# Performance work log

Hardware: AMD Instinct MI355X
Metric: run time of the kernel (lower is better)

Reference implementation:

```python
import jax, jax.numpy as jnp
import numpy as np

B, N = 64, 128
SELF_DIM, AGENT_DIM = 6, 7
C = 32            # in_mlp_dims[-1] == ia_mlp_dims[-1]
GRU_H = 2 * C     # 64
DN = ('NCHW', 'OIHW', 'NCHW')


def _lin(key, out_d, in_d):
    k1, k2 = jax.random.split(key)
    s = 1.0 / np.sqrt(in_d)
    w = jax.random.uniform(k1, (out_d, in_d), minval=-s, maxval=s, dtype=jnp.float32)
    b = jax.random.uniform(k2, (out_d,), minval=-s, maxval=s, dtype=jnp.float32)
    return w, b


def setup_inputs() -> dict:
    ks = jax.random.split(jax.random.key(0), 20)
    d = {}
    d['state'] = jax.random.normal(ks[0], (B, N, SELF_DIM + AGENT_DIM), jnp.float32)
    d['w_in1'], d['b_in1'] = _lin(ks[1], 64, AGENT_DIM)
    d['w_in2'], d['b_in2'] = _lin(ks[2], C, 64)
    s1 = 1.0 / np.sqrt(C * 9)
    d['w_c1'] = jax.random.uniform(ks[3], (64, C, 3, 3), minval=-s1, maxval=s1, dtype=jnp.float32)
    d['b_c1'] = jnp.zeros((64,), jnp.float32)
    s2 = 1.0 / np.sqrt(64 * 9)
    d['w_c2'] = jax.random.uniform(ks[4], (C, 64, 3, 3), minval=-s2, maxval=s2, dtype=jnp.float32)
    d['b_c2'] = jnp.zeros((C,), jnp.float32)
    d['w_ia1'], d['b_ia1'] = _lin(ks[5], 64, C)
    d['w_ia2'], d['b_ia2'] = _lin(ks[6], C, 64)
    d['w_s1'], d['b_s1'] = _lin(ks[7], 64, C + SELF_DIM)
    d['w_s2'], d['b_s2'] = _lin(ks[8], 32, 64)
    d['w_a1'], d['b_a1'] = _lin(ks[9], 64, 64)
    d['w_a2'], d['b_a2'] = _lin(ks[10], 32, 64)
    d['w_a3'], d['b_a3'] = _lin(ks[11], 1, 32)
    d['w_z'], _ = _lin(ks[12], GRU_H, 2 * GRU_H)
    d['w_r'], _ = _lin(ks[13], GRU_H, 2 * GRU_H)
    d['w_q'], _ = _lin(ks[14], GRU_H, 2 * GRU_H)
    d['w_m1'], d['b_m1'] = _lin(ks[15], 128, GRU_H + SELF_DIM)
    d['w_m2'], d['b_m2'] = _lin(ks[16], 64, 128)
    d['w_m3'], d['b_m3'] = _lin(ks[17], 1, 64)
    return d


def _forward(state, w_in1, b_in1, w_in2, b_in2, w_c1, b_c1, w_c2, b_c2,
             w_ia1, b_ia1, w_ia2, b_ia2, w_s1, b_s1, w_s2, b_s2,
             w_a1, b_a1, w_a2, b_a2, w_a3, b_a3, w_z, w_r, w_q,
             w_m1, b_m1, w_m2, b_m2, w_m3, b_m3):
    self_state = state[:, :, :SELF_DIM]            # (B, N, 6)
    agents = state[:, :, SELF_DIM:]                # (B, N, 7)

    # input_mlp (last_relu=True)
    h = jax.nn.relu(agents @ w_in1.T + b_in1)
    in_out = jax.nn.relu(h @ w_in2.T + b_in2)      # (B, N, C)

    # ---- AFAModule: pairwise N x N construction + conv2d edge-MLP + softmax agg ----
    f = in_out.transpose(0, 2, 1)                  # (B, C, N)
    eye = jnp.eye(N, dtype=f.dtype)
    # pair[b,c,i,j] = f[b,c,i] - f[b,c,j] + f[b,c,i]*delta_ij
    pair = f[:, :, :, None] - f[:, :, None, :] + f[:, :, :, None] * eye  # (B, C, N, N)
    w = jax.lax.conv_general_dilated(pair, w_c1, (1, 1), 'SAME', dimension_numbers=DN)
    w = jax.nn.relu(w + b_c1[None, :, None, None])
    w = jax.lax.conv_general_dilated(w, w_c2, (1, 1), 'SAME', dimension_numbers=DN)
    w = w + b_c2[None, :, None, None]
    w = jax.nn.softmax(w, axis=-1)
    afa = (pair * w).sum(-1)                        # (B, C, N)
    afa = afa.reshape(B, N, C)                      # faithful to torch .view (no transpose)
    x = in_out + afa

    # ia_mlp
    h1 = jax.nn.relu(x @ w_ia1.T + b_ia1)
    ia = h1 @ w_ia2.T + b_ia2                       # (B, N, C)

    # sort_mlp
    sort_in = jnp.concatenate([ia, self_state], axis=-1)  # (B, N, C+6)
    s1 = jax.nn.relu(sort_in @ w_s1.T + b_s1)
    sort_out = s1 @ w_s2.T + b_s2                   # (B, N, 32)
    gstate = jnp.broadcast_to(jnp.mean(sort_out, 1, keepdims=True), (B, N, 32))
    sort_mlp_input = jnp.concatenate([sort_out, gstate], axis=-1)  # (B, N, 64)

    # attention scores with masked-exp normalization
    a1 = jax.nn.relu(sort_mlp_input @ w_a1.T + b_a1)
    a2 = jax.nn.relu(a1 @ w_a2.T + b_a2)
    scores = (a2 @ w_a3.T + b_a3)[..., 0]           # (B, N)
    scores_exp = jnp.exp(scores) * (scores != 0).astype(scores.dtype)
    weights = (scores_exp / jnp.sum(scores_exp, 1, keepdims=True))[..., None]
    weighted = weights * sort_mlp_input             # (B, N, 64)

    # custom conv1d GRU (kernel 1, no bias -> channel matmuls)
    gru_input = weighted.reshape(B, GRU_H, N)       # faithful to torch .view
    h0 = sort_mlp_input.transpose(0, 2, 1)          # (B, 64, N)
    hx = jnp.concatenate([h0, gru_input], axis=1)   # (B, 128, N)
    z = jax.nn.sigmoid(jnp.einsum('oc,bcn->bon', w_z, hx))
    r = jax.nn.sigmoid(jnp.einsum('oc,bcn->bon', w_r, hx))
    q = jnp.tanh(jnp.einsum('oc,bcn->bon', w_q, jnp.concatenate([r * h0, gru_input], axis=1)))
    hn = (1 - z) * h0 + z * q
    hn = jnp.mean(hn, axis=2)                       # (B, 64)

    joint = jnp.concatenate([self_state[:, 0, :], hn], axis=1)  # (B, 70)
    m1 = jax.nn.relu(joint @ w_m1.T + b_m1)
    m2 = jax.nn.relu(m1 @ w_m2.T + b_m2)
    value = m2 @ w_m3.T + b_m3
    return value.reshape(B, -1)


def reference(state, w_in1, b_in1, w_in2, b_in2, w_c1, b_c1, w_c2, b_c2,
              w_ia1, b_ia1, w_ia2, b_ia2, w_s1, b_s1, w_s2, b_s2,
              w_a1, b_a1, w_a2, b_a2, w_a3, b_a3, w_z, w_r, w_q,
              w_m1, b_m1, w_m2, b_m2, w_m3, b_m3):
    return _forward(state, w_in1, b_in1, w_in2, b_in2, w_c1, b_c1, w_c2, b_c2,
                    w_ia1, b_ia1, w_ia2, b_ia2, w_s1, b_s1, w_s2, b_s2,
                    w_a1, b_a1, w_a2, b_a2, w_a3, b_a3, w_z, w_r, w_q,
                    w_m1, b_m1, w_m2, b_m2, w_m3, b_m3)
```

## Files before the change

### kernel.cpp

```cpp
#include <hip/hip_runtime.h>
#include <math.h>


typedef short bf16x8 __attribute__((ext_vector_type(8)));
typedef float f32x16 __attribute__((ext_vector_type(16)));

__device__ inline unsigned int bf16_rne(float x) {
  unsigned int u = __float_as_uint(x);
  return (u + 0x7fffu + ((u >> 16) & 1u)) >> 16;
}

__device__ inline unsigned int pk_bf16(float a, float b) {
  unsigned int r;
  asm("v_cvt_pk_bf16_f32 %0, %1, %2" : "=v"(r) : "v"(a), "v"(b));
  return r;
}

#define MF(A, B, Cc) __builtin_amdgcn_mfma_f32_32x32x16_bf16((A), (B), (Cc), 0, 0, 0)

__global__ __launch_bounds__(128) void k1_front(
    const float* __restrict__ state, const float* __restrict__ w_in1,
    const float* __restrict__ b_in1, const float* __restrict__ w_in2,
    const float* __restrict__ b_in2, float* __restrict__ f,
    const float* __restrict__ w_c2, unsigned short* __restrict__ Apack) {
// ... 52 lines not shown
  __syncthreads();
  if (t < 32) {
    int c = t;
#pragma unroll
    for (int di = 0; di < 3; di++) {
      float w0 = w1s[c * 9 + di * 3 + 0], w1 = w1s[c * 9 + di * 3 + 1],
            w2 = w1s[c * 9 + di * 3 + 2];
      wrow[(c * 3 + di) * 3 + 0] = w1 + w2;
      wrow[(c * 3 + di) * 3 + 1] = w0 + w1 + w2;
      wrow[(c * 3 + di) * 3 + 2] = w0 + w1;
    }
#pragma unroll
    for (int dj = 0; dj < 3; dj++) {
      float w0 = w1s[c * 9 + 0 * 3 + dj], w1 = w1s[c * 9 + 1 * 3 + dj],
            w2 = w1s[c * 9 + 2 * 3 + dj];
      wcol[(c * 3 + dj) * 3 + 0] = w1 + w2;
      wcol[(c * 3 + dj) * 3 + 1] = w0 + w1 + w2;
      wcol[(c * 3 + dj) * 3 + 2] = w0 + w1;
    }
  }
  __syncthreads();
  int i = t;
  float r0 = 0, r1 = 0, r2 = 0, c0 = 0, c1 = 0, c2 = 0;
  float d0 = 0, d1 = 0, d2 = 0, d3 = 0, d4 = 0;
  for (int c = 0; c < 32; c++) {
    float fm = (i >= 1) ? fL[c * 128 + i - 1] : 0.f;
    float f0 = fL[c * 128 + i];
    float fp = (i < 127) ? fL[c * 128 + i + 1] : 0.f;
    const float* wr = &wrow[c * 9];
    r0 += fm * wr[0] + f0 * wr[3] + fp * wr[6];
    r1 += fm * wr[1] + f0 * wr[4] + fp * wr[7];
    r2 += fm * wr[2] + f0 * wr[5] + fp * wr[8];
    const float* wc = &wcol[c * 9];
    c0 += fm * wc[0] + f0 * wc[3] + fp * wc[6];
    c1 += fm * wc[1] + f0 * wc[4] + fp * wc[7];
    c2 += fm * wc[2] + f0 * wc[5] + fp * wc[8];
    const float* wp = &w1s[c * 9];
    d0 += fm * wp[2];
    d1 += fm * wp[1] + f0 * wp[5];
    d2 += fm * wp[0] + f0 * wp[4] + fp * wp[8];
    d3 += f0 * wp[3] + fp * wp[7];
    d4 += fp * wp[6];
  }
  R[((b * 3 + 0) * 64 + o) * 128 + i] = r0;
  R[((b * 3 + 1) * 64 + o) * 128 + i] = r1;
  R[((b * 3 + 2) * 64 + o) * 128 + i] = r2;
  C[((b * 3 + 0) * 64 + o) * 128 + i] = c0;
  C[((b * 3 + 1) * 64 + o) * 128 + i] = c1;
  C[((b * 3 + 2) * 64 + o) * 128 + i] = c2;
  float* dp = &D[((b * 64 + o) * 128 + i) * 5];
  dp[0] = d0; dp[1] = d1; dp[2] = d2; dp[3] = d3; dp[4] = d4;
}

__global__ __launch_bounds__(512, 4) void k3_conv2(
    const float* __restrict__ f, const float* __restrict__ R,
    const float* __restrict__ C, const float* __restrict__ D,
    const float* __restrict__ b_c1, const unsigned short* __restrict__ Apack,
    const float* __restrict__ b_c2, float* __restrict__ afa) {
  extern __shared__ unsigned short G[];
  int iblk = blockIdx.x, b = blockIdx.y, t = threadIdx.x;
  int i0 = iblk * 2;
  int lane = t & 63, wv = t >> 6;
  int jt = wv & 3, cg = wv >> 2;
  int nn = lane & 31;
  int ccoff_half = (lane >> 5) * 8;
  const bf16x8* A8 = (const bf16x8*)Apack;
  bf16x8 zero8 = {0, 0, 0, 0, 0, 0, 0, 0};
  f32x16 acc0 = {0, 0, 0, 0, 0, 0, 0, 0, 0, 0, 0, 0, 0, 0, 0, 0};
  f32x16 acc1 = {0, 0, 0, 0, 0, 0, 0, 0, 0, 0, 0, 0, 0, 0, 0, 0};

  int ipl = t >> 7;
  int sh = (t >> 6) & 1;
  int cpr = (t >> 2) & 15;
  int q = t & 3;
  int j0r = q * 32;
  int ip = i0 - 1 + ipl;
  bool rowok = (ip >= 0 && ip <= 127);
  int ipc = ip < 0 ? 0 : (ip > 127 ? 127 : ip);
  int ic = (ipc == 0) ? 0 : ((ipc == 127) ? 2 : 1);

  int ipl2 = t / 80;
  int rem2 = t % 80;
  int jw2 = rem2 >> 4;
  int ccp2 = rem2 & 15;
  int ip2 = i0 - 1 + ipl2;

  for (int half = 0; half < 2; half++) {
    if (half) __syncthreads();
    {
      int cc = half * 32 + cpr * 2;
      float bias0 = b_c1[cc], bias1 = b_c1[cc + 1];
      float base0 = R[((b * 3 + 1) * 64 + cc) * 128 + ipc] + bias0;
      float base1 = R[((b * 3 + 1) * 64 + cc + 1) * 128 + ipc] + bias1;
      float r0v0 = 0, r0v1 = 0, r2v0 = 0, r2v1 = 0;
      if (q == 0 && sh == 0) {
        r0v0 = R[((b * 3 + 0) * 64 + cc) * 128 + ipc] + bias0;
        r0v1 = R[((b * 3 + 0) * 64 + cc + 1) * 128 + ipc] + bias1;
      }
      if (q == 3 && sh == 1) {
        r2v0 = R[((b * 3 + 2) * 64 + cc) * 128 + ipc] + bias0;
        r2v1 = R[((b * 3 + 2) * 64 + cc + 1) * 128 + ipc] + bias1;
      }
      const float* C0 = &C[((b * 3 + ic) * 64 + cc) * 128 + j0r];
      const float* C1 = C0 + 128;
      unsigned int gbase = (unsigned)((ipl * 128 + j0r) * 40 + 2 * cpr);
#pragma unroll
      for (int u = 0; u < 4; u++) {
        int s4 = (sh * 4 + u + q) & 7;
        float4 c0 = ((const float4*)C0)[s4];
        float4 c1 = ((const float4*)C1)[s4];
        float v0[4], v1[4];
        v0[0] = base0 - c0.x; v0[1] = base0 - c0.y;
        v0[2] = base0 - c0.z; v0[3] = base0 - c0.w;
        v1[0] = base1 - c1.x; v1[1] = base1 - c1.y;
        v1[2] = base1 - c1.z; v1[3] = base1 - c1.w;
        if (q == 0 && s4 == 0) { v0[0] = r0v0 - c0.x; v1[0] = r0v1 - c1.x; }
        if (q == 3 && s4 == 7) { v0[3] = r2v0 - c0.w; v1[3] = r2v1 - c1.w; }
#pragma unroll
        for (int k = 0; k < 4; k++) {
          float a0 = rowok ? fmaxf(v0[k], 0.f) : 0.f;
          float a1 = rowok ? fmaxf(v1[k], 0.f) : 0.f;
          unsigned int hw = pk_bf16(a0, a1);
          float h0f = __uint_as_float(hw << 16);
          float h1f = __uint_as_float(hw & 0xffff0000u);
          unsigned int lw = pk_bf16(a0 - h0f, a1 - h1f);
          unsigned int off = gbase + (unsigned)((s4 * 4 + k) * 40);
          *(unsigned int*)&G[off] = hw;
          *(unsigned int*)&G[off + 20480] = lw;
        }
      }
    }
    __syncthreads();
    if (t < 320 && ip2 >= 0 && ip2 <= 127) {
      int j2 = ip2 - 2 + jw2;
      if (j2 >= 0 && j2 <= 127) {
        int cc2 = half * 32 + ccp2 * 2;
        int ic2 = (ip2 == 0) ? 0 : ((ip2 == 127) ? 2 : 1);
        int jsel = (j2 == 0) ? 0 : ((j2 == 127) ? 2 : 1);
        float b0 = b_c1[cc2], b1 = b_c1[cc2 + 1];
        float bb0 = R[((b * 3 + jsel) * 64 + cc2) * 128 + ip2] + b0;
        float bb1 = R[((b * 3 + jsel) * 64 + cc2 + 1) * 128 + ip2] + b1;
        float cv0 = C[((b * 3 + ic2) * 64 + cc2) * 128 + j2];
        float cv1 = C[((b * 3 + ic2) * 64 + cc2 + 1) * 128 + j2];
        float dv0 = D[((b * 64 + cc2) * 128 + ip2) * 5 + jw2];
        float dv1 = D[((b * 64 + cc2 + 1) * 128 + ip2) * 5 + jw2];
        float a0 = fmaxf(bb0 - cv0 + dv0, 0.f);
        float a1 = fmaxf(bb1 - cv1 + dv1, 0.f);
        unsigned int hw = pk_bf16(a0, a1);
        float h0f = __uint_as_float(hw << 16);
        float h1f = __uint_as_float(hw & 0xffff0000u);
        unsigned int lw = pk_bf16(a0 - h0f, a1 - h1f);
        unsigned int off = (unsigned)((ipl2 * 128 + j2) * 40 + 2 * ccp2);
        *(unsigned int*)&G[off] = hw;
        *(unsigned int*)&G[off + 20480] = lw;
      }
    }
    __syncthreads();
    {
      int chunk = half * 2 + cg;
      bf16x8 Ah[9], Al[9];
#pragma unroll
      for (int rx = 0; rx < 9; rx++) {
        Ah[rx] = A8[(rx * 4 + chunk) * 64 + lane];
        Al[rx] = A8[((9 + rx) * 4 + chunk) * 64 + lane];
      }
      int ccoff = cg * 16 + ccoff_half;
#pragma unroll
      for (int rowidx = 0; rowidx < 4; rowidx++) {
#pragma unroll
        for (int x = 0; x < 3; x++) {
          int imgj = jt * 32 + nn + x - 1;
          int ij = imgj < 0 ? 0 : (imgj > 127 ? 127 : imgj);
          int off = (rowidx * 128 + ij) * 40 + ccoff;
          bf16x8 bh = *(const bf16x8*)&G[off];
          bf16x8 bl = *(const bf16x8*)&G[off + 20480];
          if (imgj < 0 || imgj > 127) { bh = zero8; bl = zero8; }
          if (rowidx == 0) {
            acc0 = MF(Ah[x], bh, acc0);
            acc0 = MF(Ah[x], bl, acc0);
            acc0 = MF(Al[x], bh, acc0);
          } else if (rowidx == 1) {
            acc0 = MF(Ah[3 + x], bh, acc0);
            acc0 = MF(Ah[3 + x], bl, acc0);
            acc0 = MF(Al[3 + x], bh, acc0);
            acc1 = MF(Ah[x], bh, acc1);
            acc1 = MF(Ah[x], bl, acc1);
            acc1 = MF(Al[x], bh, acc1);
          } else if (rowidx == 2) {
            acc0 = MF(Ah[6 + x], bh, acc0);
            acc0 = MF(Ah[6 + x], bl, acc0);
            acc0 = MF(Al[6 + x], bh, acc0);
            acc1 = MF(Ah[3 + x], bh, acc1);
            acc1 = MF(Ah[3 + x], bl, acc1);
            acc1 = MF(Al[3 + x], bh, acc1);
          } else {
            acc1 = MF(Ah[6 + x], bh, acc1);
            acc1 = MF(Ah[6 + x], bl, acc1);
            acc1 = MF(Al[6 + x], bh, acc1);
          }
        }
      }
    }
  }
  __syncthreads();
  const int LSTR = 129;
  float* logits = (float*)G;
  float* fbuf = (float*)G + 64 * LSTR;
  int j = jt * 32 + nn;
  if (cg == 0) {
#pragma unroll
    for (int reg = 0; reg < 16; reg++) {
      int o2 = (reg & 3) + 8 * (reg >> 2) + 4 * (lane >> 5);
      logits[(0 * 32 + o2) * LSTR + j] = acc0[reg];
      logits[(1 * 32 + o2) * LSTR + j] = acc1[reg];
    }
  } else {
    for (int idx = t - 256; idx < 1024; idx += 256) {
      float4 v = ((const float4*)(f + b * 4096))[idx];
      int c = idx >> 5, s4f = idx & 31;
      float* dst = &fbuf[c * LSTR + s4f * 4];
      dst[0] = v.x; dst[1] = v.y; dst[2] = v.z; dst[3] = v.w;
    }
  }
  __syncthreads();
  if (cg == 1) {
#pragma unroll
    for (int reg = 0; reg < 16; reg++) {
      int o2 = (reg & 3) + 8 * (reg >> 2) + 4 * (lane >> 5);
      logits[(0 * 32 + o2) * LSTR + j] += acc0[reg];
      logits[(1 * 32 + o2) * LSTR + j] += acc1[reg];
    }
  }
  __syncthreads();
  {
    int i2 = t >> 8;
    int o2e = (t >> 3) & 31;
    int qe = t & 7;
    int rot = (qe * 2) & 15;
    const float* lrow = &logits[(i2 * 32 + o2e) * LSTR + qe * 16];
    float bias2 = b_c2[o2e];
    float vals[16];
    float mx = -3.0e38f;
#pragma unroll
    for (int s = 0; s < 16; s++) {
      vals[s] = lrow[(s + rot) & 15] + bias2;
      mx = fmaxf(mx, vals[s]);
    }
    mx = fmaxf(mx, __shfl_xor(mx, 1));
    mx = fmaxf(mx, __shfl_xor(mx, 2));
    mx = fmaxf(mx, __shfl_xor(mx, 4));
    float sum = 0.f;
#pragma unroll
    for (int s = 0; s < 16; s++) {
      vals[s] = expf(vals[s] - mx);
      sum += vals[s];
    }
    sum += __shfl_xor(sum, 1);
    sum += __shfl_xor(sum, 2);
    sum += __shfl_xor(sum, 4);
    float inv = 1.f / sum;
    int gi = i0 + i2;
    float fi = fbuf[o2e * LSTR + gi];
    float part = 0.f;
#pragma unroll
    for (int s = 0; s < 16; s++) {
      int jj = qe * 16 + ((s + rot) & 15);
      float w = vals[s] * inv;
      part += w * (fi - fbuf[o2e * LSTR + jj]);
      if (jj == gi) part += w * fi;
    }
    part += __shfl_xor(part, 1);
    part += __shfl_xor(part, 2);
    part += __shfl_xor(part, 4);
    if (qe == 0) afa[(b * 32 + o2e) * 128 + gi] = part;
  }
}

__global__ __launch_bounds__(256) void k4a_sort(
    const float* __restrict__ state, const float* __restrict__ f,
    const float* __restrict__ afa, const float* __restrict__ w_ia1,
    const float* __restrict__ b_ia1, const float* __restrict__ w_ia2,
    const float* __restrict__ b_ia2, const float* __restrict__ w_s1,
    const float* __restrict__ b_s1, const float* __restrict__ w_s2,
    const float* __restrict__ b_s2, float* __restrict__ so_g) {
  int blk = blockIdx.x;
  int b = blk >> 2, nq = blk & 3;
  int t = threadIdx.x, row = t >> 3, lane = t & 7;
  int n = nq * 32 + row;
  __shared__ float bufA[32][40];
  __shared__ float bufB[32][72];
  {
    int c0 = lane * 4;
    float4 av = *(const float4*)&afa[b * 4096 + n * 32 + c0];
    bufA[row][c0 + 0] = f[b * 4096 + (c0 + 0) * 128 + n] + av.x;
    bufA[row][c0 + 1] = f[b * 4096 + (c0 + 1) * 128 + n] + av.y;
    bufA[row][c0 + 2] = f[b * 4096 + (c0 + 2) * 128 + n] + av.z;
    bufA[row][c0 + 3] = f[b * 4096 + (c0 + 3) * 128 + n] + av.w;
  }
  __syncthreads();
#pragma unroll
  for (int oi = 0; oi < 8; oi++) {
    int o = lane * 8 + oi;
    float a = b_ia1[o];
#pragma unroll 8
    for (int c = 0; c < 32; c++) a += w_ia1[o * 32 + c] * bufA[row][c];
    bufB[row][o] = fmaxf(a, 0.f);
  }
  __syncthreads();
  {
    float r0[4];
#pragma unroll
    for (int oi = 0; oi < 4; oi++) {
      int o = lane * 4 + oi;
      float a = b_ia2[o];
#pragma unroll 8
      for (int k = 0; k < 64; k++) a += w_ia2[o * 64 + k] * bufB[row][k];
      r0[oi] = a;
    }
    __syncthreads();
#pragma unroll
    for (int oi = 0; oi < 4; oi++) bufA[row][lane * 4 + oi] = r0[oi];
    if (lane == 0) {
#pragma unroll
      for (int k = 0; k < 6; k++)
        bufA[row][32 + k] = state[(b * 128 + n) * 13 + k];
    }
  }
  __syncthreads();
#pragma unroll
  for (int oi = 0; oi < 8; oi++) {
    int o = lane * 8 + oi;
    float a = b_s1[o];
#pragma unroll 2
    for (int k = 0; k < 38; k++) a += w_s1[o * 38 + k] * bufA[row][k];
    bufB[row][o] = fmaxf(a, 0.f);
  }
  __syncthreads();
#pragma unroll
  for (int oi = 0; oi < 4; oi++) {
    int o = lane * 4 + oi;
    float a = b_s2[o];
#pragma unroll 8
    for (int k = 0; k < 64; k++) a += w_s2[o * 64 + k] * bufB[row][k];
    so_g[(b * 128 + n) * 32 + o] = a;
  }
}

__global__ __launch_bounds__(256) void k4c_attn(
    const float* __restrict__ so_g, const float* __restrict__ w_a1,
    const float* __restrict__ b_a1, const float* __restrict__ w_a2,
    const float* __restrict__ b_a2, const float* __restrict__ w_a3,
    const float* __restrict__ b_a3, float* __restrict__ smi,
    float* __restrict__ se_g) {
  int blk = blockIdx.x;
  int b = blk >> 2, nq = blk & 3;
  int t = threadIdx.x, row = t >> 3, lane = t & 7;
  int n = nq * 32 + row;
  __shared__ float bufA[32][72];
  __shared__ float bufB[32][72];
  __shared__ float gred[8][32];
  __shared__ float gs_s[32];
  {
    int c = t & 31, grp = t >> 5;
    float s = 0.f;
#pragma unroll 4
    for (int k = 0; k < 16; k++) s += so_g[(b * 128 + grp * 16 + k) * 32 + c];
    gred[grp][c] = s;
  }
  {
    int c0 = lane * 4;
    float4 sv = *(const float4*)&so_g[(b * 128 + n) * 32 + c0];
    *(float4*)&bufA[row][c0] = sv;
    *(float4*)&smi[b * 8192 + n * 64 + c0] = sv;
  }
  __syncthreads();
  if (t < 32) {
    float s = 0.f;
#pragma unroll
    for (int g = 0; g < 8; g++) s += gred[g][t];
    gs_s[t] = s * (1.f / 128.f);
  }
  __syncthreads();
  {
    int c0 = lane * 4;
    float4 gv = *(const float4*)&gs_s[c0];
    *(float4*)&bufA[row][32 + c0] = gv;
    *(float4*)&smi[b * 8192 + n * 64 + 32 + c0] = gv;
  }
  __syncthreads();
#pragma unroll
  for (int oi = 0; oi < 8; oi++) {
    int o = lane * 8 + oi;
    float a = b_a1[o];
#pragma unroll 8
    for (int k = 0; k < 64; k++) a += w_a1[o * 64 + k] * bufA[row][k];
    bufB[row][o] = fmaxf(a, 0.f);
  }
  __syncthreads();
  float ps = 0.f;
#pragma unroll
  for (int oi = 0; oi < 4; oi++) {
    int o = lane * 4 + oi;
    float a = b_a2[o];
#pragma unroll 8
    for (int k = 0; k < 64; k++) a += w_a2[o * 64 + k] * bufB[row][k];
    ps += w_a3[o] * fmaxf(a, 0.f);
  }
  for (int d = 4; d >= 1; d >>= 1) ps += __shfl_xor(ps, d, 8);
  if (lane == 0) {
    float sc = ps + b_a3[0];
    se_g[b * 128 + n] = (sc != 0.f) ? expf(sc) : 0.f;
  }
}

__global__ __launch_bounds__(256) void k5a_r(
    const float* __restrict__ smi, const float* __restrict__ se_g,
    const float* __restrict__ w_r, float* __restrict__ rh) {
  int cch = blockIdx.x, b = blockIdx.y, t = threadIdx.x;
  __shared__ float smi_s[128 * 65];
  __shared__ float wts_s[128];
  __shared__ float invs_s;
  for (int idx = t; idx < 8192; idx += 256) {
    int n = idx >> 6, k = idx & 63;
    smi_s[n * 65 + k] = smi[b * 8192 + idx];
  }
  if (t < 128) wts_s[t] = se_g[b * 128 + t];
  __syncthreads();
  if (t < 64) {
    float s2 = wts_s[t] + wts_s[t + 64];
    for (int d = 32; d >= 1; d >>= 1) s2 += __shfl_xor(s2, d);
    if (t == 0) invs_s = 1.f / s2;
  }
  __syncthreads();
  if (t < 128) wts_s[t] *= invs_s;
  __syncthreads();
  int c = cch * 16 + (t >> 4), l = t & 15;
  float accs[8];
#pragma unroll
  for (int m = 0; m < 8; m++) accs[m] = 0.f;
  const float* wr = &w_r[c * 128];
  for (int k = 0; k < 64; k++) {
    float wv = wr[k];
#pragma unroll
    for (int m = 0; m < 8; m++) accs[m] += wv * smi_s[(l + 16 * m) * 65 + k];
  }
  for (int c2 = 0; c2 < 64; c2++) {
    float wv = wr[64 + c2];
    float g0 = wts_s[2 * c2], g1 = wts_s[2 * c2 + 1];
#pragma unroll
    for (int m = 0; m < 8; m++) {
      int nb = (m >> 2) & 1, nl = l + 16 * (m & 3);
      accs[m] += wv * ((nb ? g1 : g0) * smi_s[(2 * c2 + nb) * 65 + nl]);
    }
  }
#pragma unroll
  for (int m = 0; m < 8; m++) {
    int n = l + 16 * m;
    float r = 1.f / (1.f + expf(-accs[m]));
    rh[(b * 64 + c) * 128 + n] = r * smi_s[n * 65 + c];
  }
}

__global__ __launch_bounds__(256) void k5b_gru(
    const float* __restrict__ smi, const float* __restrict__ se_g,
    const float* __restrict__ rh, const float* __restrict__ w_z,
    const float* __restrict__ w_q, float* __restrict__ hnm) {
  int och = blockIdx.x, b = blockIdx.y, t = threadIdx.x;
  __shared__ float smi_s[128 * 65];
  __shared__ float wts_s[128];
  __shared__ float invs_s;
  for (int idx = t; idx < 8192; idx += 256) {
    int n = idx >> 6, k = idx & 63;
    smi_s[n * 65 + k] = smi[b * 8192 + idx];
  }
  if (t < 128) wts_s[t] = se_g[b * 128 + t];
  __syncthreads();
  if (t < 64) {
    float s2 = wts_s[t] + wts_s[t + 64];
    for (int d = 32; d >= 1; d >>= 1) s2 += __shfl_xor(s2, d);
    if (t == 0) invs_s = 1.f / s2;
  }
  __syncthreads();
  if (t < 128) wts_s[t] *= invs_s;
  __syncthreads();
  int o = och * 16 + (t >> 4), l = t & 15;
  float az[8], aq[8];
#pragma unroll
  for (int m = 0; m < 8; m++) { az[m] = 0.f; aq[m] = 0.f; }
  const float* wz = &w_z[o * 128];
  const float* wq = &w_q[o * 128];
  const float* rhb = rh + b * 8192;
  for (int k = 0; k < 64; k++) {
    float wv = wz[k];
#pragma unroll
    for (int m = 0; m < 8; m++) az[m] += wv * smi_s[(l + 16 * m) * 65 + k];
  }
  for (int c = 0; c < 64; c++) {
    float wv = wq[c];
#pragma unroll
    for (int m = 0; m < 8; m++) aq[m] += wv * rhb[c * 128 + l + 16 * m];
  }
  for (int c2 = 0; c2 < 64; c2++) {
    float wvz = wz[64 + c2], wvq = wq[64 + c2];
    float g0 = wts_s[2 * c2], g1 = wts_s[2 * c2 + 1];
#pragma unroll
    for (int m = 0; m < 8; m++) {
      int nb = (m >> 2) & 1, nl = l + 16 * (m & 3);
      float gin = (nb ? g1 : g0) * smi_s[(2 * c2 + nb) * 65 + nl];
      az[m] += wvz * gin;
      aq[m] += wvq * gin;
    }
  }
  float part = 0.f;
#pragma unroll
  for (int m = 0; m < 8; m++) {
    int n = l + 16 * m;
    float z = 1.f / (1.f + expf(-az[m]));
    float q = tanhf(aq[m]);
    float h0 = smi_s[n * 65 + o];
    part += (1.f - z) * h0 + z * q;
  }
  for (int d = 8; d >= 1; d >>= 1) part += __shfl_xor(part, d, 16);
  if (l == 0) hnm[b * 64 + o] = part * (1.f / 128.f);
}

__global__ __launch_bounds__(128, 1) void k6_head(
    const float* __restrict__ state, const float* __restrict__ hnm,
    const float* __restrict__ w_m1, const float* __restrict__ b_m1,
    const float* __restrict__ w_m2, const float* __restrict__ b_m2,
    const float* __restrict__ w_m3, const float* __restrict__ b_m3,
    float* __restrict__ out) {
  int b = blockIdx.x, t = threadIdx.x;
  __shared__ float joint[70];
  __shared__ float m1s[128];
  __shared__ float red[64];
  if (t < 6) joint[t] = state[b * 1664 + t];
  if (t < 64) joint[6 + t] = hnm[b * 64 + t];
  __syncthreads();
  float a = b_m1[t];
#pragma unroll 2
  for (int k = 0; k < 70; k++) a += w_m1[t * 70 + k] * joint[k];
  m1s[t] = fmaxf(a, 0.f);
  __syncthreads();
  if (t < 64) {
    float a2 = b_m2[t];
#pragma unroll 8
    for (int k = 0; k < 128; k++) a2 += w_m2[t * 128 + k] * m1s[k];
    red[t] = fmaxf(a2, 0.f) * w_m3[t];
  }
  __syncthreads();
  for (int s = 32; s >= 1; s >>= 1) {
    if (t < s) red[t] += red[t + s];
    __syncthreads();
  }
  if (t == 0) out[b] = red[0] + b_m3[0];
}

extern "C" void kernel_launch(void* const* d_in, const int* in_sizes, int n_in,
                              void* d_out, int out_size, void* d_ws, size_t ws_size,
                              hipStream_t stream) {
  const float* state = (const float*)d_in[0];
  const float* w_in1 = (const float*)d_in[1];
  const float* b_in1 = (const float*)d_in[2];
  const float* w_in2 = (const float*)d_in[3];
  const float* b_in2 = (const float*)d_in[4];
  const float* w_c1  = (const float*)d_in[5];
  const float* b_c1  = (const float*)d_in[6];
  const float* w_c2  = (const float*)d_in[7];
  const float* b_c2  = (const float*)d_in[8];
  const float* w_ia1 = (const float*)d_in[9];
  const float* b_ia1 = (const float*)d_in[10];
  const float* w_ia2 = (const float*)d_in[11];
  const float* b_ia2 = (const float*)d_in[12];
  const float* w_s1  = (const float*)d_in[13];
  const float* b_s1  = (const float*)d_in[14];
  const float* w_s2  = (const float*)d_in[15];
  const float* b_s2  = (const float*)d_in[16];
  const float* w_a1  = (const float*)d_in[17];
  const float* b_a1  = (const float*)d_in[18];
  const float* w_a2  = (const float*)d_in[19];
  const float* b_a2  = (const float*)d_in[20];
  const float* w_a3  = (const float*)d_in[21];
  const float* b_a3  = (const float*)d_in[22];
  const float* w_z   = (const float*)d_in[23];
  const float* w_r   = (const float*)d_in[24];
  const float* w_q   = (const float*)d_in[25];
  const float* w_m1  = (const float*)d_in[26];
  const float* b_m1  = (const float*)d_in[27];
  const float* w_m2  = (const float*)d_in[28];
  const float* b_m2  = (const float*)d_in[29];
  const float* w_m3  = (const float*)d_in[30];
  const float* b_m3  = (const float*)d_in[31];
  float* ws    = (float*)d_ws;
  float* f_    = ws;
  float* R_    = ws + 262144;
  float* C_    = ws + 1835008;
  float* D_    = ws + 3407872;
  float* afa_  = ws + 6029312;
  float* smi_  = ws + 6291456;
  float* rh_   = ws + 6823936;
  float* hnm_  = ws + 7348224;
  unsigned short* Apack_ = (unsigned short*)(ws + 7352320);
  float* so_   = ws + 7376896;
  float* se_   = ws + 7641088;
  float* out   = (float*)d_out;

  k1_front<<<dim3(64, 5), 128, 0, stream>>>(state, w_in1, b_in1, w_in2, b_in2,
                                            f_, w_c2, Apack_);
  k2_pre<<<dim3(64, 64), 128, 0, stream>>>(f_, w_c1, R_, C_, D_);
  k3_conv2<<<dim3(64, 64), 512, 81920, stream>>>(f_, R_, C_, D_, b_c1, Apack_,
                                                 b_c2, afa_);
  k4a_sort<<<256, 256, 0, stream>>>(state, f_, afa_, w_ia1, b_ia1, w_ia2, b_ia2,
                                    w_s1, b_s1, w_s2, b_s2, so_);
  k4c_attn<<<256, 256, 0, stream>>>(so_, w_a1, b_a1, w_a2, b_a2, w_a3, b_a3,
                                    smi_, se_);
  k5a_r<<<dim3(4, 64), 256, 0, stream>>>(smi_, se_, w_r, rh_);
  k5b_gru<<<dim3(4, 64), 256, 0, stream>>>(smi_, se_, rh_, w_z, w_q, hnm_);
  k6_head<<<64, 128, 0, stream>>>(state, hnm_, w_m1, b_m1, w_m2, b_m2, w_m3,
                                  b_m3, out);
}
```

Baseline: 436.3 us.

## Halve conv2 LDS by quarter-channel staging and per-row wave split

Restructures k3_conv2 to stage 16 channels at a time in four passes instead of 32 channels in two, halving the LDS buffer. Each wave group now owns one output row instead of splitting channels and reducing both rows, which removes the two-phase accumulate into shared memory. The f tile is read straight from global instead of being staged in LDS. It also swaps expf for __expf and raises the launch-bounds block hint to fit more blocks per CU. The cost is more barriers, weight fragments reloaded from global each pass, and slightly lower exp accuracy.

```diff
diff --git a/kernel.cpp b/kernel.cpp
--- a/kernel.cpp
+++ b/kernel.cpp
@@ -128,7 +128,7 @@
   dp[0] = d0; dp[1] = d1; dp[2] = d2; dp[3] = d3; dp[4] = d4;
 }
 
-__global__ __launch_bounds__(512, 4) void k3_conv2(
+__global__ __launch_bounds__(512, 8) void k3_conv2(
     const float* __restrict__ f, const float* __restrict__ R,
     const float* __restrict__ C, const float* __restrict__ D,
     const float* __restrict__ b_c1, const unsigned short* __restrict__ Apack,
@@ -139,15 +139,14 @@
   int lane = t & 63, wv = t >> 6;
   int jt = wv & 3, cg = wv >> 2;
   int nn = lane & 31;
-  int ccoff_half = (lane >> 5) * 8;
+  int kgoff = (lane >> 5) * 8;
   const bf16x8* A8 = (const bf16x8*)Apack;
   bf16x8 zero8 = {0, 0, 0, 0, 0, 0, 0, 0};
-  f32x16 acc0 = {0, 0, 0, 0, 0, 0, 0, 0, 0, 0, 0, 0, 0, 0, 0, 0};
-  f32x16 acc1 = {0, 0, 0, 0, 0, 0, 0, 0, 0, 0, 0, 0, 0, 0, 0, 0};
+  f32x16 acc = {0, 0, 0, 0, 0, 0, 0, 0, 0, 0, 0, 0, 0, 0, 0, 0};
 
   int ipl = t >> 7;
-  int sh = (t >> 6) & 1;
-  int cpr = (t >> 2) & 15;
+  int sq = (t >> 5) & 3;
+  int cpr = (t >> 2) & 7;
   int q = t & 3;
   int j0r = q * 32;
   int ip = i0 - 1 + ipl;
@@ -155,34 +154,34 @@
   int ipc = ip < 0 ? 0 : (ip > 127 ? 127 : ip);
   int ic = (ipc == 0) ? 0 : ((ipc == 127) ? 2 : 1);
 
-  int ipl2 = t / 80;
-  int rem2 = t % 80;
-  int jw2 = rem2 >> 4;
-  int ccp2 = rem2 & 15;
+  int ipl2 = t / 40;
+  int rem2 = t % 40;
+  int jw2 = rem2 >> 3;
+  int ccp2 = rem2 & 7;
   int ip2 = i0 - 1 + ipl2;
 
-  for (int half = 0; half < 2; half++) {
-    if (half) __syncthreads();
+  for (int qtr = 0; qtr < 4; qtr++) {
+    if (qtr) __syncthreads();
     {
-      int cc = half * 32 + cpr * 2;
+      int cc = qtr * 16 + cpr * 2;
       float bias0 = b_c1[cc], bias1 = b_c1[cc + 1];
       float base0 = R[((b * 3 + 1) * 64 + cc) * 128 + ipc] + bias0;
       float base1 = R[((b * 3 + 1) * 64 + cc + 1) * 128 + ipc] + bias1;
       float r0v0 = 0, r0v1 = 0, r2v0 = 0, r2v1 = 0;
-      if (q == 0 && sh == 0) {
+      if (q == 0 && sq == 0) {
         r0v0 = R[((b * 3 + 0) * 64 + cc) * 128 + ipc] + bias0;
         r0v1 = R[((b * 3 + 0) * 64 + cc + 1) * 128 + ipc] + bias1;
       }
-      if (q == 3 && sh == 1) {
+      if (q == 3 && sq == 2) {
         r2v0 = R[((b * 3 + 2) * 64 + cc) * 128 + ipc] + bias0;
         r2v1 = R[((b * 3 + 2) * 64 + cc + 1) * 128 + ipc] + bias1;
       }
       const float* C0 = &C[((b * 3 + ic) * 64 + cc) * 128 + j0r];
       const float* C1 = C0 + 128;
-      unsigned int gbase = (unsigned)((ipl * 128 + j0r) * 40 + 2 * cpr);
-#pragma unroll
-      for (int u = 0; u < 4; u++) {
-        int s4 = (sh * 4 + u + q) & 7;
+      unsigned int gbase = (unsigned)((ipl * 128 + j0r) * 20 + 2 * cpr);
+#pragma unroll
+      for (int u = 0; u < 2; u++) {
+        int s4 = (sq * 2 + u + q) & 7;
         float4 c0 = ((const float4*)C0)[s4];
         float4 c1 = ((const float4*)C1)[s4];
         float v0[4], v1[4];
@@ -200,17 +199,17 @@
           float h0f = __uint_as_float(hw << 16);
           float h1f = __uint_as_float(hw & 0xffff0000u);
           unsigned int lw = pk_bf16(a0 - h0f, a1 - h1f);
-          unsigned int off = gbase + (unsigned)((s4 * 4 + k) * 40);
+          unsigned int off = gbase + (unsigned)((s4 * 4 + k) * 20);
           *(unsigned int*)&G[off] = hw;
-          *(unsigned int*)&G[off + 20480] = lw;
+          *(unsigned int*)&G[off + 10240] = lw;
         }
       }
     }
     __syncthreads();
-    if (t < 320 && ip2 >= 0 && ip2 <= 127) {
+    if (t < 160 && ip2 >= 0 && ip2 <= 127) {
       int j2 = ip2 - 2 + jw2;
       if (j2 >= 0 && j2 <= 127) {
-        int cc2 = half * 32 + ccp2 * 2;
+        int cc2 = qtr * 16 + ccp2 * 2;
         int ic2 = (ip2 == 0) ? 0 : ((ip2 == 127) ? 2 : 1);
         int jsel = (j2 == 0) ? 0 : ((j2 == 127) ? 2 : 1);
         float b0 = b_c1[cc2], b1 = b_c1[cc2 + 1];
@@ -226,54 +225,29 @@
         float h0f = __uint_as_float(hw << 16);
         float h1f = __uint_as_float(hw & 0xffff0000u);
         unsigned int lw = pk_bf16(a0 - h0f, a1 - h1f);
-        unsigned int off = (unsigned)((ipl2 * 128 + j2) * 40 + 2 * ccp2);
+        unsigned int off = (unsigned)((ipl2 * 128 + j2) * 20 + 2 * ccp2);
         *(unsigned int*)&G[off] = hw;
-        *(unsigned int*)&G[off + 20480] = lw;
+        *(unsigned int*)&G[off + 10240] = lw;
       }
     }
     __syncthreads();
     {
-      int chunk = half * 2 + cg;
-      bf16x8 Ah[9], Al[9];
-#pragma unroll
-      for (int rx = 0; rx < 9; rx++) {
-        Ah[rx] = A8[(rx * 4 + chunk) * 64 + lane];
-        Al[rx] = A8[((9 + rx) * 4 + chunk) * 64 + lane];
-      }
-      int ccoff = cg * 16 + ccoff_half;
-#pragma unroll
-      for (int rowidx = 0; rowidx < 4; rowidx++) {
+#pragma unroll
+      for (int rr = 0; rr < 3; rr++) {
+        int rowidx = cg + rr;
 #pragma unroll
         for (int x = 0; x < 3; x++) {
+          bf16x8 ah = A8[((rr * 3 + x) * 4 + qtr) * 64 + lane];
+          bf16x8 al = A8[((9 + rr * 3 + x) * 4 + qtr) * 64 + lane];
           int imgj = jt * 32 + nn + x - 1;
           int ij = imgj < 0 ? 0 : (imgj > 127 ? 127 : imgj);
-          int off = (rowidx * 128 + ij) * 40 + ccoff;
+          int off = (rowidx * 128 + ij) * 20 + kgoff;
           bf16x8 bh = *(const bf16x8*)&G[off];
-          bf16x8 bl = *(const bf16x8*)&G[off + 20480];
+          bf16x8 bl = *(const bf16x8*)&G[off + 10240];
           if (imgj < 0 || imgj > 127) { bh = zero8; bl = zero8; }
-          if (rowidx == 0) {
-            acc0 = MF(Ah[x], bh, acc0);
-            acc0 = MF(Ah[x], bl, acc0);
-            acc0 = MF(Al[x], bh, acc0);
-          } else if (rowidx == 1) {
-            acc0 = MF(Ah[3 + x], bh, acc0);
-            acc0 = MF(Ah[3 + x], bl, acc0);
-            acc0 = MF(Al[3 + x], bh, acc0);
-            acc1 = MF(Ah[x], bh, acc1);
-            acc1 = MF(Ah[x], bl, acc1);
-            acc1 = MF(Al[x], bh, acc1);
-          } else if (rowidx == 2) {
-            acc0 = MF(Ah[6 + x], bh, acc0);
-            acc0 = MF(Ah[6 + x], bl, acc0);
-            acc0 = MF(Al[6 + x], bh, acc0);
-            acc1 = MF(Ah[3 + x], bh, acc1);
-            acc1 = MF(Ah[3 + x], bl, acc1);
-            acc1 = MF(Al[3 + x], bh, acc1);
-          } else {
-            acc1 = MF(Ah[6 + x], bh, acc1);
-            acc1 = MF(Ah[6 + x], bl, acc1);
-            acc1 = MF(Al[6 + x], bh, acc1);
-          }
+          acc = MF(ah, bh, acc);
+          acc = MF(ah, bl, acc);
+          acc = MF(al, bh, acc);
         }
       }
     }
@@ -281,31 +255,11 @@
   __syncthreads();
   const int LSTR = 129;
   float* logits = (float*)G;
-  float* fbuf = (float*)G + 64 * LSTR;
   int j = jt * 32 + nn;
-  if (cg == 0) {
-#pragma unroll
-    for (int reg = 0; reg < 16; reg++) {
-      int o2 = (reg & 3) + 8 * (reg >> 2) + 4 * (lane >> 5);
-      logits[(0 * 32 + o2) * LSTR + j] = acc0[reg];
-      logits[(1 * 32 + o2) * LSTR + j] = acc1[reg];
-    }
-  } else {
-    for (int idx = t - 256; idx < 1024; idx += 256) {
-      float4 v = ((const float4*)(f + b * 4096))[idx];
-      int c = idx >> 5, s4f = idx & 31;
-      float* dst = &fbuf[c * LSTR + s4f * 4];
-      dst[0] = v.x; dst[1] = v.y; dst[2] = v.z; dst[3] = v.w;
-    }
-  }
-  __syncthreads();
-  if (cg == 1) {
-#pragma unroll
-    for (int reg = 0; reg < 16; reg++) {
-      int o2 = (reg & 3) + 8 * (reg >> 2) + 4 * (lane >> 5);
-      logits[(0 * 32 + o2) * LSTR + j] += acc0[reg];
-      logits[(1 * 32 + o2) * LSTR + j] += acc1[reg];
-    }
+#pragma unroll
+  for (int reg = 0; reg < 16; reg++) {
+    int o2 = (reg & 3) + 8 * (reg >> 2) + 4 * (lane >> 5);
+    logits[(cg * 32 + o2) * LSTR + j] = acc[reg];
   }
   __syncthreads();
   {
@@ -314,6 +268,7 @@
     int qe = t & 7;
     int rot = (qe * 2) & 15;
     const float* lrow = &logits[(i2 * 32 + o2e) * LSTR + qe * 16];
+    const float* frow = &f[b * 4096 + o2e * 128];
     float bias2 = b_c2[o2e];
     float vals[16];
     float mx = -3.0e38f;
@@ -328,7 +283,7 @@
     float sum = 0.f;
 #pragma unroll
     for (int s = 0; s < 16; s++) {
-      vals[s] = expf(vals[s] - mx);
+      vals[s] = __expf(vals[s] - mx);
       sum += vals[s];
     }
     sum += __shfl_xor(sum, 1);
@@ -336,13 +291,13 @@
     sum += __shfl_xor(sum, 4);
     float inv = 1.f / sum;
     int gi = i0 + i2;
-    float fi = fbuf[o2e * LSTR + gi];
+    float fi = frow[gi];
     float part = 0.f;
 #pragma unroll
     for (int s = 0; s < 16; s++) {
       int jj = qe * 16 + ((s + rot) & 15);
       float w = vals[s] * inv;
-      part += w * (fi - fbuf[o2e * LSTR + jj]);
+      part += w * (fi - frow[jj]);
       if (jj == gi) part += w * fi;
     }
     part += __shfl_xor(part, 1);
@@ -684,7 +639,7 @@
   k1_front<<<dim3(64, 5), 128, 0, stream>>>(state, w_in1, b_in1, w_in2, b_in2,
                                             f_, w_c2, Apack_);
   k2_pre<<<dim3(64, 64), 128, 0, stream>>>(f_, w_c1, R_, C_, D_);
-  k3_conv2<<<dim3(64, 64), 512, 81920, stream>>>(f_, R_, C_, D_, b_c1, Apack_,
+  k3_conv2<<<dim3(64, 64), 512, 40960, stream>>>(f_, R_, C_, D_, b_c1, Apack_,
                                                  b_c2, afa_);
   k4a_sort<<<256, 256, 0, stream>>>(state, f_, afa_, w_ia1, b_ia1, w_ia2, b_ia2,
                                     w_s1, b_s1, w_s2, b_s2, so_);
```

New measurement: 620.5 us. 42.2% more time.

## Fuse post-conv MLP, attention, GRU and head into one per-batch kernel

Applied to the files above, without the earlier changes.

Replaces five tail kernels (sort MLP, attention, GRU r-gate, GRU z/q, head) with a single kernel that runs one 1024-thread block per batch element and keeps every intermediate in shared memory. This removes four launches and the global round trips for so, smi, se, rh and hnm. In exchange it uses only 64 blocks, each needing about 96 KB of LDS, so parallelism drops from 256 blocks to 64 for the GRU stages, and rh aliases the bufA/bufB region.

```diff
diff --git a/kernel.cpp b/kernel.cpp
--- a/kernel.cpp
+++ b/kernel.cpp
@@ -352,26 +352,43 @@
   }
 }
 
-__global__ __launch_bounds__(256) void k4a_sort(
+__global__ __launch_bounds__(1024, 1) void k4_fused(
     const float* __restrict__ state, const float* __restrict__ f,
     const float* __restrict__ afa, const float* __restrict__ w_ia1,
     const float* __restrict__ b_ia1, const float* __restrict__ w_ia2,
     const float* __restrict__ b_ia2, const float* __restrict__ w_s1,
     const float* __restrict__ b_s1, const float* __restrict__ w_s2,
-    const float* __restrict__ b_s2, float* __restrict__ so_g) {
-  int blk = blockIdx.x;
-  int b = blk >> 2, nq = blk & 3;
-  int t = threadIdx.x, row = t >> 3, lane = t & 7;
-  int n = nq * 32 + row;
-  __shared__ float bufA[32][40];
-  __shared__ float bufB[32][72];
+    const float* __restrict__ b_s2, const float* __restrict__ w_a1,
+    const float* __restrict__ b_a1, const float* __restrict__ w_a2,
+    const float* __restrict__ b_a2, const float* __restrict__ w_a3,
+    const float* __restrict__ b_a3, const float* __restrict__ w_r,
+    const float* __restrict__ w_z, const float* __restrict__ w_q,
+    const float* __restrict__ w_m1, const float* __restrict__ b_m1,
+    const float* __restrict__ w_m2, const float* __restrict__ b_m2,
+    const float* __restrict__ w_m3, const float* __restrict__ b_m3,
+    float* __restrict__ out) {
+  extern __shared__ float P[];
+  float* smi = P;
+  float* wts = P + 8320;
+  float* gred = P + 8448;
+  float* gs = P + 9472;
+  float* hnm = P + 9504;
+  float* invp = P + 9568;
+  float* jnt = P + 9600;
+  float* bufA = P + 9728;
+  float* bufB = P + 9728 + 5120;
+  float* rh = P + 9728;
+
+  int b = blockIdx.x, t = threadIdx.x;
+  int n = t >> 3, lane = t & 7;
+
   {
     int c0 = lane * 4;
     float4 av = *(const float4*)&afa[b * 4096 + n * 32 + c0];
-    bufA[row][c0 + 0] = f[b * 4096 + (c0 + 0) * 128 + n] + av.x;
-    bufA[row][c0 + 1] = f[b * 4096 + (c0 + 1) * 128 + n] + av.y;
-    bufA[row][c0 + 2] = f[b * 4096 + (c0 + 2) * 128 + n] + av.z;
-    bufA[row][c0 + 3] = f[b * 4096 + (c0 + 3) * 128 + n] + av.w;
+    bufA[n * 40 + c0 + 0] = f[b * 4096 + (c0 + 0) * 128 + n] + av.x;
+    bufA[n * 40 + c0 + 1] = f[b * 4096 + (c0 + 1) * 128 + n] + av.y;
+    bufA[n * 40 + c0 + 2] = f[b * 4096 + (c0 + 2) * 128 + n] + av.z;
+    bufA[n * 40 + c0 + 3] = f[b * 4096 + (c0 + 3) * 128 + n] + av.w;
   }
   __syncthreads();
 #pragma unroll
@@ -379,8 +396,8 @@
     int o = lane * 8 + oi;
     float a = b_ia1[o];
 #pragma unroll 8
-    for (int c = 0; c < 32; c++) a += w_ia1[o * 32 + c] * bufA[row][c];
-    bufB[row][o] = fmaxf(a, 0.f);
+    for (int c = 0; c < 32; c++) a += w_ia1[o * 32 + c] * bufA[n * 40 + c];
+    bufB[n * 72 + o] = fmaxf(a, 0.f);
   }
   __syncthreads();
   {
@@ -390,16 +407,16 @@
       int o = lane * 4 + oi;
       float a = b_ia2[o];
 #pragma unroll 8
-      for (int k = 0; k < 64; k++) a += w_ia2[o * 64 + k] * bufB[row][k];
+      for (int k = 0; k < 64; k++) a += w_ia2[o * 64 + k] * bufB[n * 72 + k];
       r0[oi] = a;
     }
     __syncthreads();
 #pragma unroll
-    for (int oi = 0; oi < 4; oi++) bufA[row][lane * 4 + oi] = r0[oi];
+    for (int oi = 0; oi < 4; oi++) bufA[n * 40 + lane * 4 + oi] = r0[oi];
     if (lane == 0) {
 #pragma unroll
       for (int k = 0; k < 6; k++)
-        bufA[row][32 + k] = state[(b * 128 + n) * 13 + k];
+        bufA[n * 40 + 32 + k] = state[(b * 128 + n) * 13 + k];
     }
   }
   __syncthreads();
@@ -408,8 +425,8 @@
     int o = lane * 8 + oi;
     float a = b_s1[o];
 #pragma unroll 2
-    for (int k = 0; k < 38; k++) a += w_s1[o * 38 + k] * bufA[row][k];
-    bufB[row][o] = fmaxf(a, 0.f);
+    for (int k = 0; k < 38; k++) a += w_s1[o * 38 + k] * bufA[n * 40 + k];
+    bufB[n * 72 + o] = fmaxf(a, 0.f);
   }
   __syncthreads();
 #pragma unroll
@@ -417,51 +434,28 @@
     int o = lane * 4 + oi;
     float a = b_s2[o];
 #pragma unroll 8
-    for (int k = 0; k < 64; k++) a += w_s2[o * 64 + k] * bufB[row][k];
-    so_g[(b * 128 + n) * 32 + o] = a;
-  }
-}
-
-__global__ __launch_bounds__(256) void k4c_attn(
-    const float* __restrict__ so_g, const float* __restrict__ w_a1,
-    const float* __restrict__ b_a1, const float* __restrict__ w_a2,
-    const float* __restrict__ b_a2, const float* __restrict__ w_a3,
-    const float* __restrict__ b_a3, float* __restrict__ smi,
-    float* __restrict__ se_g) {
-  int blk = blockIdx.x;
-  int b = blk >> 2, nq = blk & 3;
-  int t = threadIdx.x, row = t >> 3, lane = t & 7;
-  int n = nq * 32 + row;
-  __shared__ float bufA[32][72];
-  __shared__ float bufB[32][72];
-  __shared__ float gred[8][32];
-  __shared__ float gs_s[32];
+    for (int k = 0; k < 64; k++) a += w_s2[o * 64 + k] * bufB[n * 72 + k];
+    smi[n * 65 + o] = a;
+  }
+  __syncthreads();
   {
-    int c = t & 31, grp = t >> 5;
+    int c = t & 31, part = t >> 5;
     float s = 0.f;
-#pragma unroll 4
-    for (int k = 0; k < 16; k++) s += so_g[(b * 128 + grp * 16 + k) * 32 + c];
-    gred[grp][c] = s;
-  }
-  {
-    int c0 = lane * 4;
-    float4 sv = *(const float4*)&so_g[(b * 128 + n) * 32 + c0];
-    *(float4*)&bufA[row][c0] = sv;
-    *(float4*)&smi[b * 8192 + n * 64 + c0] = sv;
+#pragma unroll
+    for (int k = 0; k < 4; k++) s += smi[(part * 4 + k) * 65 + c];
+    gred[part * 32 + c] = s;
   }
   __syncthreads();
   if (t < 32) {
     float s = 0.f;
 #pragma unroll
-    for (int g = 0; g < 8; g++) s += gred[g][t];
-    gs_s[t] = s * (1.f / 128.f);
-  }
-  __syncthreads();
-  {
-    int c0 = lane * 4;
-    float4 gv = *(const float4*)&gs_s[c0];
-    *(float4*)&bufA[row][32 + c0] = gv;
-    *(float4*)&smi[b * 8192 + n * 64 + 32 + c0] = gv;
+    for (int g = 0; g < 32; g++) s += gred[g * 32 + t];
+    gs[t] = s * (1.f / 128.f);
+  }
+  __syncthreads();
+  for (int idx = t; idx < 4096; idx += 1024) {
+    int nn2 = idx >> 5, c = idx & 31;
+    smi[nn2 * 65 + 32 + c] = gs[c];
   }
   __syncthreads();
 #pragma unroll
@@ -469,167 +463,122 @@
     int o = lane * 8 + oi;
     float a = b_a1[o];
 #pragma unroll 8
-    for (int k = 0; k < 64; k++) a += w_a1[o * 64 + k] * bufA[row][k];
-    bufB[row][o] = fmaxf(a, 0.f);
-  }
-  __syncthreads();
-  float ps = 0.f;
-#pragma unroll
-  for (int oi = 0; oi < 4; oi++) {
-    int o = lane * 4 + oi;
-    float a = b_a2[o];
+    for (int k = 0; k < 64; k++) a += w_a1[o * 64 + k] * smi[n * 65 + k];
+    bufB[n * 72 + o] = fmaxf(a, 0.f);
+  }
+  __syncthreads();
+  {
+    float ps = 0.f;
+#pragma unroll
+    for (int oi = 0; oi < 4; oi++) {
+      int o = lane * 4 + oi;
+      float a = b_a2[o];
 #pragma unroll 8
-    for (int k = 0; k < 64; k++) a += w_a2[o * 64 + k] * bufB[row][k];
-    ps += w_a3[o] * fmaxf(a, 0.f);
-  }
-  for (int d = 4; d >= 1; d >>= 1) ps += __shfl_xor(ps, d, 8);
-  if (lane == 0) {
-    float sc = ps + b_a3[0];
-    se_g[b * 128 + n] = (sc != 0.f) ? expf(sc) : 0.f;
-  }
-}
-
-__global__ __launch_bounds__(256) void k5a_r(
-    const float* __restrict__ smi, const float* __restrict__ se_g,
-    const float* __restrict__ w_r, float* __restrict__ rh) {
-  int cch = blockIdx.x, b = blockIdx.y, t = threadIdx.x;
-  __shared__ float smi_s[128 * 65];
-  __shared__ float wts_s[128];
-  __shared__ float invs_s;
-  for (int idx = t; idx < 8192; idx += 256) {
-    int n = idx >> 6, k = idx & 63;
-    smi_s[n * 65 + k] = smi[b * 8192 + idx];
-  }
-  if (t < 128) wts_s[t] = se_g[b * 128 + t];
+      for (int k = 0; k < 64; k++) a += w_a2[o * 64 + k] * bufB[n * 72 + k];
+      ps += w_a3[o] * fmaxf(a, 0.f);
+    }
+    for (int d = 4; d >= 1; d >>= 1) ps += __shfl_xor(ps, d, 8);
+    if (lane == 0) {
+      float sc = ps + b_a3[0];
+      wts[n] = (sc != 0.f) ? expf(sc) : 0.f;
+    }
+  }
   __syncthreads();
   if (t < 64) {
-    float s2 = wts_s[t] + wts_s[t + 64];
+    float s2 = wts[t] + wts[t + 64];
     for (int d = 32; d >= 1; d >>= 1) s2 += __shfl_xor(s2, d);
-    if (t == 0) invs_s = 1.f / s2;
-  }
-  __syncthreads();
-  if (t < 128) wts_s[t] *= invs_s;
-  __syncthreads();
-  int c = cch * 16 + (t >> 4), l = t & 15;
-  float accs[8];
-#pragma unroll
-  for (int m = 0; m < 8; m++) accs[m] = 0.f;
-  const float* wr = &w_r[c * 128];
-  for (int k = 0; k < 64; k++) {
-    float wv = wr[k];
-#pragma unroll
-    for (int m = 0; m < 8; m++) accs[m] += wv * smi_s[(l + 16 * m) * 65 + k];
-  }
-  for (int c2 = 0; c2 < 64; c2++) {
-    float wv = wr[64 + c2];
-    float g0 = wts_s[2 * c2], g1 = wts_s[2 * c2 + 1];
+    if (t == 0) invp[0] = 1.f / s2;
+  }
+  __syncthreads();
+  if (t < 128) wts[t] *= invp[0];
+  __syncthreads();
+  {
+    int c = t >> 4, l = t & 15;
+    float accs[8];
+#pragma unroll
+    for (int m = 0; m < 8; m++) accs[m] = 0.f;
+    const float* wr = &w_r[c * 128];
+    for (int k = 0; k < 64; k++) {
+      float wv = wr[k];
+#pragma unroll
+      for (int m = 0; m < 8; m++) accs[m] += wv * smi[(l + 16 * m) * 65 + k];
+    }
+    for (int c2 = 0; c2 < 64; c2++) {
+      float wv = wr[64 + c2];
+      float g0 = wts[2 * c2], g1 = wts[2 * c2 + 1];
+#pragma unroll
+      for (int m = 0; m < 8; m++) {
+        int nb = (m >> 2) & 1, nl = l + 16 * (m & 3);
+        accs[m] += wv * ((nb ? g1 : g0) * smi[(2 * c2 + nb) * 65 + nl]);
+      }
+    }
 #pragma unroll
     for (int m = 0; m < 8; m++) {
-      int nb = (m >> 2) & 1, nl = l + 16 * (m & 3);
-      accs[m] += wv * ((nb ? g1 : g0) * smi_s[(2 * c2 + nb) * 65 + nl]);
-    }
-  }
-#pragma unroll
-  for (int m = 0; m < 8; m++) {
-    int n = l + 16 * m;
-    float r = 1.f / (1.f + expf(-accs[m]));
-    rh[(b * 64 + c) * 128 + n] = r * smi_s[n * 65 + c];
-  }
-}
-
-__global__ __launch_bounds__(256) void k5b_gru(
-    const float* __restrict__ smi, const float* __restrict__ se_g,
-    const float* __restrict__ rh, const float* __restrict__ w_z,
-    const float* __restrict__ w_q, float* __restrict__ hnm) {
-  int och = blockIdx.x, b = blockIdx.y, t = threadIdx.x;
-  __shared__ float smi_s[128 * 65];
-  __shared__ float wts_s[128];
-  __shared__ float invs_s;
-  for (int idx = t; idx < 8192; idx += 256) {
-    int n = idx >> 6, k = idx & 63;
-    smi_s[n * 65 + k] = smi[b * 8192 + idx];
-  }
-  if (t < 128) wts_s[t] = se_g[b * 128 + t];
-  __syncthreads();
-  if (t < 64) {
-    float s2 = wts_s[t] + wts_s[t + 64];
-    for (int d = 32; d >= 1; d >>= 1) s2 += __shfl_xor(s2, d);
-    if (t == 0) invs_s = 1.f / s2;
-  }
-  __syncthreads();
-  if (t < 128) wts_s[t] *= invs_s;
-  __syncthreads();
-  int o = och * 16 + (t >> 4), l = t & 15;
-  float az[8], aq[8];
-#pragma unroll
-  for (int m = 0; m < 8; m++) { az[m] = 0.f; aq[m] = 0.f; }
-  const float* wz = &w_z[o * 128];
-  const float* wq = &w_q[o * 128];
-  const float* rhb = rh + b * 8192;
-  for (int k = 0; k < 64; k++) {
-    float wv = wz[k];
-#pragma unroll
-    for (int m = 0; m < 8; m++) az[m] += wv * smi_s[(l + 16 * m) * 65 + k];
-  }
-  for (int c = 0; c < 64; c++) {
-    float wv = wq[c];
-#pragma unroll
-    for (int m = 0; m < 8; m++) aq[m] += wv * rhb[c * 128 + l + 16 * m];
-  }
-  for (int c2 = 0; c2 < 64; c2++) {
-    float wvz = wz[64 + c2], wvq = wq[64 + c2];
-    float g0 = wts_s[2 * c2], g1 = wts_s[2 * c2 + 1];
+      int nn2 = l + 16 * m;
+      float r = 1.f / (1.f + expf(-accs[m]));
+      rh[c * 128 + nn2] = r * smi[nn2 * 65 + c];
+    }
+  }
+  __syncthreads();
+  {
+    int o = t >> 4, l = t & 15;
+    float az[8], aq[8];
+#pragma unroll
+    for (int m = 0; m < 8; m++) { az[m] = 0.f; aq[m] = 0.f; }
+    const float* wz = &w_z[o * 128];
+    const float* wq = &w_q[o * 128];
+    for (int k = 0; k < 64; k++) {
+      float wv = wz[k];
+#pragma unroll
+      for (int m = 0; m < 8; m++) az[m] += wv * smi[(l + 16 * m) * 65 + k];
+    }
+    for (int c = 0; c < 64; c++) {
+      float wv = wq[c];
+#pragma unroll
+      for (int m = 0; m < 8; m++) aq[m] += wv * rh[c * 128 + l + 16 * m];
+    }
+    for (int c2 = 0; c2 < 64; c2++) {
+      float wvz = wz[64 + c2], wvq = wq[64 + c2];
+      float g0 = wts[2 * c2], g1 = wts[2 * c2 + 1];
+#pragma unroll
+      for (int m = 0; m < 8; m++) {
+        int nb = (m >> 2) & 1, nl = l + 16 * (m & 3);
+        float gin = (nb ? g1 : g0) * smi[(2 * c2 + nb) * 65 + nl];
+        az[m] += wvz * gin;
+        aq[m] += wvq * gin;
+      }
+    }
+    float part = 0.f;
 #pragma unroll
     for (int m = 0; m < 8; m++) {
-      int nb = (m >> 2) & 1, nl = l + 16 * (m & 3);
-      float gin = (nb ? g1 : g0) * smi_s[(2 * c2 + nb) * 65 + nl];
-      az[m] += wvz * gin;
-      aq[m] += wvq * gin;
-    }
-  }
-  float part = 0.f;
-#pragma unroll
-  for (int m = 0; m < 8; m++) {
-    int n = l + 16 * m;
-    float z = 1.f / (1.f + expf(-az[m]));
-    float q = tanhf(aq[m]);
-    float h0 = smi_s[n * 65 + o];
-    part += (1.f - z) * h0 + z * q;
-  }
-  for (int d = 8; d >= 1; d >>= 1) part += __shfl_xor(part, d, 16);
-  if (l == 0) hnm[b * 64 + o] = part * (1.f / 128.f);
-}
-
-__global__ __launch_bounds__(128, 1) void k6_head(
-    const float* __restrict__ state, const float* __restrict__ hnm,
-    const float* __restrict__ w_m1, const float* __restrict__ b_m1,
-    const float* __restrict__ w_m2, const float* __restrict__ b_m2,
-    const float* __restrict__ w_m3, const float* __restrict__ b_m3,
-    float* __restrict__ out) {
-  int b = blockIdx.x, t = threadIdx.x;
-  __shared__ float joint[70];
-  __shared__ float m1s[128];
-  __shared__ float red[64];
-  if (t < 6) joint[t] = state[b * 1664 + t];
-  if (t < 64) joint[6 + t] = hnm[b * 64 + t];
-  __syncthreads();
-  float a = b_m1[t];
+      int nn2 = l + 16 * m;
+      float z = 1.f / (1.f + expf(-az[m]));
+      float qv = tanhf(aq[m]);
+      float h0 = smi[nn2 * 65 + o];
+      part += (1.f - z) * h0 + z * qv;
+    }
+    for (int d = 8; d >= 1; d >>= 1) part += __shfl_xor(part, d, 16);
+    if (l == 0) hnm[o] = part * (1.f / 128.f);
+  }
+  __syncthreads();
+  if (t < 6) jnt[t] = state[b * 1664 + t];
+  if (t < 64) jnt[6 + t] = hnm[t];
+  __syncthreads();
+  if (t < 128) {
+    float a = b_m1[t];
 #pragma unroll 2
-  for (int k = 0; k < 70; k++) a += w_m1[t * 70 + k] * joint[k];
-  m1s[t] = fmaxf(a, 0.f);
+    for (int k = 0; k < 70; k++) a += w_m1[t * 70 + k] * jnt[k];
+    gred[t] = fmaxf(a, 0.f);
+  }
   __syncthreads();
   if (t < 64) {
     float a2 = b_m2[t];
 #pragma unroll 8
-    for (int k = 0; k < 128; k++) a2 += w_m2[t * 128 + k] * m1s[k];
-    red[t] = fmaxf(a2, 0.f) * w_m3[t];
-  }
-  __syncthreads();
-  for (int s = 32; s >= 1; s >>= 1) {
-    if (t < s) red[t] += red[t + s];
-    __syncthreads();
-  }
-  if (t == 0) out[b] = red[0] + b_m3[0];
+    for (int k = 0; k < 128; k++) a2 += w_m2[t * 128 + k] * gred[k];
+    float v = fmaxf(a2, 0.f) * w_m3[t];
+    for (int d = 32; d >= 1; d >>= 1) v += __shfl_xor(v, d);
+    if (t == 0) out[b] = v + b_m3[0];
+  }
 }
 
 extern "C" void kernel_launch(void* const* d_in, const int* in_sizes, int n_in,
@@ -673,12 +622,7 @@
   float* C_    = ws + 1835008;
   float* D_    = ws + 3407872;
   float* afa_  = ws + 6029312;
-  float* smi_  = ws + 6291456;
-  float* rh_   = ws + 6823936;
-  float* hnm_  = ws + 7348224;
   unsigned short* Apack_ = (unsigned short*)(ws + 7352320);
-  float* so_   = ws + 7376896;
-  float* se_   = ws + 7641088;
   float* out   = (float*)d_out;
 
   k1_front<<<dim3(64, 5), 128, 0, stream>>>(state, w_in1, b_in1, w_in2, b_in2,
@@ -686,12 +630,8 @@
   k2_pre<<<dim3(64, 64), 128, 0, stream>>>(f_, w_c1, R_, C_, D_);
   k3_conv2<<<dim3(64, 64), 512, 81920, stream>>>(f_, R_, C_, D_, b_c1, Apack_,
                                                  b_c2, afa_);
-  k4a_sort<<<256, 256, 0, stream>>>(state, f_, afa_, w_ia1, b_ia1, w_ia2, b_ia2,
-                                    w_s1, b_s1, w_s2, b_s2, so_);
-  k4c_attn<<<256, 256, 0, stream>>>(so_, w_a1, b_a1, w_a2, b_a2, w_a3, b_a3,
-                                    smi_, se_);
-  k5a_r<<<dim3(4, 64), 256, 0, stream>>>(smi_, se_, w_r, rh_);
-  k5b_gru<<<dim3(4, 64), 256, 0, stream>>>(smi_, se_, rh_, w_z, w_q, hnm_);
-  k6_head<<<64, 128, 0, stream>>>(state, hnm_, w_m1, b_m1, w_m2, b_m2, w_m3,
-                                  b_m3, out);
+  k4_fused<<<64, 1024, 96256, stream>>>(
+      state, f_, afa_, w_ia1, b_ia1, w_ia2, b_ia2, w_s1, b_s1, w_s2, b_s2,
+      w_a1, b_a1, w_a2, b_a2, w_a3, b_a3, w_r, w_z, w_q, w_m1, b_m1, w_m2,
+      b_m2, w_m3, b_m3, out);
 }
```

Measured after the change: 588.5 us. +34.9%, slower.
